# Performance work log

Measured on AMD Instinct MI355X. Metric: run time of the kernel, lower is better.

Reference implementation:

```python
import jax, jax.numpy as jnp
import numpy as np

BS = 128
HW = 128
REG = 0.1


def setup_inputs() -> dict:
    key = jax.random.key(0)
    k1, k2 = jax.random.split(key)
    x1 = jax.random.normal(k1, (BS, 1, HW, HW), dtype=jnp.float32)
    x2 = jax.random.normal(k2, (BS, 1, HW, HW), dtype=jnp.float32)
    return {"x1": x1, "x2": x2}


def _calc_psd(x):
    # x: [2*bs, H, W]
    dft = jnp.fft.fft2(x)
    avgpsd = jnp.mean((dft * jnp.conj(dft)).real, axis=0)  # [H, W]
    return jnp.mean(jnp.log(avgpsd)) - jnp.log(jnp.mean(avgpsd))


def reference(x1, x2):
    a = x1[:, 0]  # [bs, H, W] (squeeze channel)
    b = x2[:, 0]
    # pairwise Frobenius distances: Dist[i, j] = ||x1[i] - x2[j]||_F
    diff = a[:, None, :, :] - b[None, :, :, :]          # [bs, bs, H, W]
    Dist = jnp.sqrt(jnp.sum(diff * diff, axis=(-2, -1)))  # [bs, bs]
    bs = Dist.shape[0]
    # CrossEntropyLoss(Dist, arange(bs)) = mean_i(logsumexp(Dist[i]) - Dist[i, i])
    log_probs = jax.nn.log_softmax(Dist, axis=-1)
    ce = -jnp.mean(jnp.diagonal(log_probs))
    # PSD regularizer on cat(x1, x2)
    x = jnp.concatenate([a, b], axis=0)  # [2*bs, H, W]
    r = _calc_psd(x)
    return ce - REG * r
```

## Files before the change

kernel.cpp:

```cpp
#include <hip/hip_runtime.h>
#include <math.h>


#define WS_N     0
#define WS_D     256
#define WS_GP    20736
#define WS_P     4215040
#define WS_PS    6344960
#define WS_PL    6345025

#define PI_F 3.14159265358979323846f

__device__ __forceinline__ void fft128_reg(float& s0r, float& s0i,
                                           float& s1r, float& s1i,
                                           float cA, float sA,
                                           const float* wr, const float* wi,
                                           int lane) {
    float er = s0r + s1r, ei = s0i + s1i;
    float dr = s0r - s1r, di = s0i - s1i;
    float orr = dr * cA - di * sA;
    float oii = dr * sA + di * cA;
    #pragma unroll
    for (int st = 0; st < 6; ++st) {
        int m = 32 >> st;
        bool up = (lane & m) == 0;
        float tr = __shfl_xor(er, m), ti = __shfl_xor(ei, m);
        float ar = tr - er, ai = ti - ei;
        float e2r = up ? (er + tr) : (ar * wr[st] - ai * wi[st]);
        float e2i = up ? (ei + ti) : (ar * wi[st] + ai * wr[st]);
        tr = __shfl_xor(orr, m); ti = __shfl_xor(oii, m);
        float br_ = tr - orr, bi_ = ti - oii;
        float o2r = up ? (orr + tr) : (br_ * wr[st] - bi_ * wi[st]);
        float o2i = up ? (oii + ti) : (br_ * wi[st] + bi_ * wr[st]);
        er = e2r; ei = e2i; orr = o2r; oii = o2i;
    }
    s0r = er; s0i = ei; s1r = orr; s1i = oii;
}

__global__ __launch_bounds__(512) void ocl_main(const float* __restrict__ x1,
                                                const float* __restrict__ x2,
                                                float* __restrict__ ws) {
    __shared__ float4 smem4[4096];
    int t = threadIdx.x;
    int bid = blockIdx.x;

    if (bid < 256) {
        float4* As = smem4;
        float4* Bs = smem4 + 2048;
        int ks = bid, k0q = ks * 16;
        const float4* A = (const float4*)x1;
        const float4* B = (const float4*)x2;
        {
            int qi = t & 15, r0 = t >> 4;
            #pragma unroll
            for (int p = 0; p < 4; ++p) {
                int r = r0 + 32 * p;
                int sq = qi ^ ((r >> 3) & 7);
                As[r * 16 + sq] = A[(size_t)r * 4096 + k0q + qi];
                Bs[r * 16 + sq] = B[(size_t)r * 4096 + k0q + qi];
            }
        }
        __syncthreads();

        int ty = t >> 4, tx = t & 15;
        float acc[4][8];
        #pragma unroll
        for (int r = 0; r < 4; ++r)
            #pragma unroll
            for (int c = 0; c < 8; ++c) acc[r][c] = 0.0f;

        for (int qk = 0; qk < 16; ++qk) {
            float4 a4[4], b4[8];
            #pragma unroll
            for (int r = 0; r < 4; ++r) {
                int rr = ty * 4 + r;
                a4[r] = As[rr * 16 + (qk ^ ((rr >> 3) & 7))];
            }
            #pragma unroll
            for (int c = 0; c < 8; ++c) {
                int rc = tx * 8 + c;
                b4[c] = Bs[rc * 16 + (qk ^ ((rc >> 3) & 7))];
            }
            #pragma unroll
            for (int r = 0; r < 4; ++r)
                #pragma unroll
                for (int c = 0; c < 8; ++c) {
                    float4 a = a4[r], b = b4[c];
                    acc[r][c] = fmaf(a.x, b.x, fmaf(a.y, b.y,
                                fmaf(a.z, b.z, fmaf(a.w, b.w, acc[r][c]))));
                }
        }

        float4* Gp4 = (float4*)(ws + WS_GP);
        #pragma unroll
        for (int r = 0; r < 4; ++r)
            #pragma unroll
            for (int cc = 0; cc < 2; ++cc) {
                int e4 = (ty * 4 + r) * 32 + tx * 2 + cc;
                Gp4[(size_t)(e4 >> 2) * 1024 + ks * 4 + (e4 & 3)] =
                    make_float4(acc[r][cc * 4 + 0], acc[r][cc * 4 + 1],
                                acc[r][cc * 4 + 2], acc[r][cc * 4 + 3]);
            }
    } else {
        float* zre = (float*)smem4;
        float* zim = zre + 8192;
        int lane = t & 63, wave = t >> 6;
        int img = bid - 256;
        const float* src = (img < 128) ? (x1 + (size_t)img * 16384)
                                       : (x2 + (size_t)(img - 128) * 16384);

        float cA, sA, wr[6], wi[6];
        {
            float th = -PI_F * (float)lane / 64.0f;
            sA = __sinf(th); cA = __cosf(th);
            #pragma unroll
            for (int st = 0; st < 6; ++st) {
                int m = 32 >> st;
                float a = -PI_F * (float)(lane & (m - 1)) / (float)m;
                wi[st] = __sinf(a); wr[st] = __cosf(a);
            }
        }
        int rb = (int)(__brev((unsigned)lane) >> 26);

        float nrm = 0.0f;
        #pragma unroll
        for (int pi = 0; pi < 8; ++pi) {
            int p = wave * 8 + pi;
            const float* r0 = src + p * 256 + lane;
            float s0r = r0[0],   s1r = r0[64];
            float s0i = r0[128], s1i = r0[192];
            nrm += s0r * s0r + s1r * s1r + s0i * s0i + s1i * s1i;
            fft128_reg(s0r, s0i, s1r, s1i, cA, sA, wr, wi, lane);
            int f0 = (2 * rb + p) & 127;
            int f1 = (2 * rb + 1 + p) & 127;
            zre[p * 128 + f0] = s0r; zim[p * 128 + f0] = s0i;
            zre[p * 128 + f1] = s1r; zim[p * 128 + f1] = s1i;
        }
        for (int off = 32; off >= 1; off >>= 1) nrm += __shfl_xor(nrm, off);
        if (lane == 0) atomicAdd(&ws[WS_N + img], nrm);
        __syncthreads();

        int p0 = (lane >> 1), p1 = 32 + (lane >> 1);
        int par = lane & 1;
        float* P = ws + WS_P;
        for (int k = wave; k < 65; k += 8) {
            float v0r, v0i, v1r, v1i;
            if (k == 0 || k == 64) {
                int c0 = (k + p0) & 127, c1 = (k + p1) & 127;
                float Z0r = zre[p0 * 128 + c0], Z0i = zim[p0 * 128 + c0];
                float Z1r = zre[p1 * 128 + c1], Z1i = zim[p1 * 128 + c1];
                v0r = par ? Z0i : Z0r; v0i = 0.0f;
                v1r = par ? Z1i : Z1r; v1i = 0.0f;
            } else {
                int kn = 128 - k;
                int ck = (k + p0) & 127, cn = (kn + p0) & 127;
                float Zkr = zre[p0 * 128 + ck], Zki = zim[p0 * 128 + ck];
                float Znr = zre[p0 * 128 + cn], Zni = zim[p0 * 128 + cn];
                float e0r = 0.5f * (Zkr + Znr), e0i = 0.5f * (Zki - Zni);
                float q0r = 0.5f * (Zki + Zni), q0i = 0.5f * (Znr - Zkr);
                v0r = par ? q0r : e0r; v0i = par ? q0i : e0i;
                ck = (k + p1) & 127; cn = (kn + p1) & 127;
                Zkr = zre[p1 * 128 + ck]; Zki = zim[p1 * 128 + ck];
                Znr = zre[p1 * 128 + cn]; Zni = zim[p1 * 128 + cn];
                float e1r = 0.5f * (Zkr + Znr), e1i = 0.5f * (Zki - Zni);
                float q1r = 0.5f * (Zki + Zni), q1i = 0.5f * (Znr - Zkr);
                v1r = par ? q1r : e1r; v1i = par ? q1i : e1i;
            }
            fft128_reg(v0r, v0i, v1r, v1i, cA, sA, wr, wi, lane);
            int m = lane & 15, hi = lane >> 4;
            P[(size_t)(k * 8 + 0 + hi) * 4096 + img * 16 + m] = v0r * v0r + v0i * v0i;
            P[(size_t)(k * 8 + 4 + hi) * 4096 + img * 16 + m] = v1r * v1r + v1i * v1i;
        }
    }
}

__global__ __launch_bounds__(256) void ocl_finish(float* __restrict__ ws) {
    int bid = blockIdx.x, t = threadIdx.x;
    int lane = t & 63, wave = t >> 6;

    if (bid < 256) {
        int g = bid;
        const float4* Gp4 = (const float4*)(ws + WS_GP);
        int q = (lane >> 4) & 3, kg = lane & 15;
        const float4* base = Gp4 + (size_t)g * 4096 + wave * 1024 + q;
        float4 v[16];
        #pragma unroll
        for (int it = 0; it < 16; ++it) v[it] = base[(kg * 16 + it) * 4];
        float4 s = v[0];
        #pragma unroll
        for (int it = 1; it < 16; ++it) {
            s.x += v[it].x; s.y += v[it].y; s.z += v[it].z; s.w += v[it].w;
        }
        #pragma unroll
        for (int msk = 1; msk <= 8; msk <<= 1) {
            s.x += __shfl_xor(s.x, msk); s.y += __shfl_xor(s.y, msk);
            s.z += __shfl_xor(s.z, msk); s.w += __shfl_xor(s.w, msk);
        }
        if (kg == 0) {
            int i = g >> 1;
            float nai = ws[WS_N + i];
            float4 nb4 = ((const float4*)(ws + WS_N + 128))[(g & 1) * 16 + wave * 4 + q];
            float4 d;
            d.x = sqrtf(fmaxf(nai + nb4.x - 2.0f * s.x, 0.0f));
            d.y = sqrtf(fmaxf(nai + nb4.y - 2.0f * s.y, 0.0f));
            d.z = sqrtf(fmaxf(nai + nb4.z - 2.0f * s.z, 0.0f));
            d.w = sqrtf(fmaxf(nai + nb4.w - 2.0f * s.w, 0.0f));
            ((float4*)(ws + WS_D))[i * 32 + (g & 1) * 16 + wave * 4 + q] = d;
        }
    } else {
        int k = bid - 256;
        const float4* P4 = (const float4*)(ws + WS_P);
        int b16 = t >> 5, m4 = (t >> 3) & 3, hq = t & 7;
        const float4* base = P4 + (size_t)(k * 8 + b16) * 1024 + m4;
        float4 s = make_float4(0.f, 0.f, 0.f, 0.f);
        #pragma unroll
        for (int half = 0; half < 2; ++half) {
            float4 u[16];
            #pragma unroll
            for (int it = 0; it < 16; ++it)
                u[it] = base[(hq * 32 + half * 16 + it) * 4];
            #pragma unroll
            for (int it = 0; it < 16; ++it) {
                s.x += u[it].x; s.y += u[it].y; s.z += u[it].z; s.w += u[it].w;
            }
        }
        #pragma unroll
        for (int msk = 1; msk <= 4; msk <<= 1) {
            s.x += __shfl_xor(s.x, msk); s.y += __shfl_xor(s.y, msk);
            s.z += __shfl_xor(s.z, msk); s.w += __shfl_xor(s.w, msk);
        }
        float sS = 0.0f, sL = 0.0f;
        if (hq == 0) {
            float w = (k == 0 || k == 64) ? 1.0f : 2.0f;
            sS = w * (s.x + s.y + s.z + s.w);
            sL = w * (logf(s.x) + logf(s.y) + logf(s.z) + logf(s.w));
        }
        #pragma unroll
        for (int off = 32; off >= 1; off >>= 1) {
            sS += __shfl_xor(sS, off);
            sL += __shfl_xor(sL, off);
        }
        __shared__ float aS[4], aL[4];
        if (lane == 0) { aS[wave] = sS; aL[wave] = sL; }
        __syncthreads();
        if (t == 0) {
            ws[WS_PS + k] = aS[0] + aS[1] + aS[2] + aS[3];
            ws[WS_PL + k] = aL[0] + aL[1] + aL[2] + aL[3];
        }
    }
}

__global__ __launch_bounds__(256) void ocl_tail(const float* __restrict__ ws,
                                                float* __restrict__ out) {
    int t = threadIdx.x, lane = t & 63, wave = t >> 6;

    int i = t >> 1, h = t & 1;
    const float4* D4 = (const float4*)(ws + WS_D);
    float4 dv[16];
    #pragma unroll
    for (int it = 0; it < 16; ++it) dv[it] = D4[i * 32 + h * 16 + it];
    float mx = -1.0f;
    #pragma unroll
    for (int it = 0; it < 16; ++it)
        mx = fmaxf(mx, fmaxf(fmaxf(dv[it].x, dv[it].y), fmaxf(dv[it].z, dv[it].w)));
    float mo = __shfl_xor(mx, 1);
    float m2 = fmaxf(mx, mo);
    float sm = 0.0f;
    #pragma unroll
    for (int it = 0; it < 16; ++it)
        sm += __expf(dv[it].x - m2) + __expf(dv[it].y - m2) +
              __expf(dv[it].z - m2) + __expf(dv[it].w - m2);
    sm += __shfl_xor(sm, 1);
    float dii = 0.0f;
    if ((i >> 6) == h) {
        int lc = i & 63;
        float4 dq = dv[lc >> 2];
        dii = (i & 2) ? ((i & 1) ? dq.w : dq.z) : ((i & 1) ? dq.y : dq.x);
    }
    dii += __shfl_xor(dii, 1);
    float rowacc = 0.5f * (m2 + logf(sm) - dii);

    float sS = 0.0f, sL = 0.0f;
    if (t < 65) { sS = ws[WS_PS + t]; sL = ws[WS_PL + t]; }
    #pragma unroll
    for (int off = 32; off >= 1; off >>= 1) {
        sS += __shfl_xor(sS, off);
        sL += __shfl_xor(sL, off);
        rowacc += __shfl_xor(rowacc, off);
    }
    __shared__ float bS[4], bL[4], bR[4];
    if (lane == 0) { bS[wave] = sS; bL[wave] = sL; bR[wave] = rowacc; }
    __syncthreads();
    if (t == 0) {
        float S_ = bS[0] + bS[1] + bS[2] + bS[3];
        float L_ = bL[0] + bL[1] + bL[2] + bL[3];
        float R_ = bR[0] + bR[1] + bR[2] + bR[3];
        float ce = R_ / 128.0f;
        float r  = L_ / 16384.0f - logf(S_ / 16384.0f);
        out[0] = ce - 0.1f * r;
    }
}

extern "C" void kernel_launch(void* const* d_in, const int* in_sizes, int n_in,
                              void* d_out, int out_size, void* d_ws, size_t ws_size,
                              hipStream_t stream) {
    (void)in_sizes; (void)n_in; (void)out_size; (void)ws_size;
    const float* x1 = (const float*)d_in[0];
    const float* x2 = (const float*)d_in[1];
    float* ws  = (float*)d_ws;
    float* out = (float*)d_out;

    hipLaunchKernelGGL(ocl_main,   dim3(512), dim3(512), 0, stream, x1, x2, ws);
    hipLaunchKernelGGL(ocl_finish, dim3(321), dim3(256), 0, stream, ws);
    hipLaunchKernelGGL(ocl_tail,   dim3(1),   dim3(256), 0, stream, ws, out);
}
```

Baseline: 100.3 us.

## Replace norm atomics with per-wave partials and fuse partial softmax into finish

The FFT kernel now writes one squared-norm partial per wave instead of doing an atomicAdd per image, and the finish kernel sums those partials itself. The finish kernel also computes the distance tile, takes a per-block max and sum-of-exp, and records the diagonal entry. The tail kernel then only merges two partial log-sum-exp values per row. This removes the atomics, their need for a zeroed accumulator, and the tail's serial row scan over the full distance matrix. In exchange the finish blocks gain extra syncthreads and shared-memory reductions.

Result: faster. 94.28 us (-6.0%).

```diff
diff --git a/kernel.cpp b/kernel.cpp
--- a/kernel.cpp
+++ b/kernel.cpp
@@ -2,8 +2,10 @@
 #include <math.h>
 
 
-#define WS_N     0
-#define WS_D     256
+#define WS_SE    256
+#define WS_MX    512
+#define WS_DII   768
+#define WS_NP    16640
 #define WS_GP    20736
 #define WS_P     4215040
 #define WS_PS    6344960
@@ -137,7 +139,7 @@
             zre[p * 128 + f1] = s1r; zim[p * 128 + f1] = s1i;
         }
         for (int off = 32; off >= 1; off >>= 1) nrm += __shfl_xor(nrm, off);
-        if (lane == 0) atomicAdd(&ws[WS_N + img], nrm);
+        if (lane == 0) ws[WS_NP + img * 8 + wave] = nrm;
         __syncthreads();
 
         int p0 = (lane >> 1), p1 = 32 + (lane >> 1);
@@ -186,6 +188,21 @@
         float4 v[16];
         #pragma unroll
         for (int it = 0; it < 16; ++it) v[it] = base[(kg * 16 + it) * 4];
+
+        __shared__ float nbs[64];
+        __shared__ float s_na;
+        __shared__ float sm[4], sm2[4];
+        if (t < 64) {
+            const float* np = ws + WS_NP + (size_t)(128 + (g & 1) * 64 + t) * 8;
+            nbs[t] = ((np[0] + np[1]) + (np[2] + np[3])) +
+                     ((np[4] + np[5]) + (np[6] + np[7]));
+        }
+        if (t == 64) {
+            const float* np = ws + WS_NP + (size_t)(g >> 1) * 8;
+            s_na = ((np[0] + np[1]) + (np[2] + np[3])) +
+                   ((np[4] + np[5]) + (np[6] + np[7]));
+        }
+
         float4 s = v[0];
         #pragma unroll
         for (int it = 1; it < 16; ++it) {
@@ -196,16 +213,39 @@
             s.x += __shfl_xor(s.x, msk); s.y += __shfl_xor(s.y, msk);
             s.z += __shfl_xor(s.z, msk); s.w += __shfl_xor(s.w, msk);
         }
-        if (kg == 0) {
-            int i = g >> 1;
-            float nai = ws[WS_N + i];
-            float4 nb4 = ((const float4*)(ws + WS_N + 128))[(g & 1) * 16 + wave * 4 + q];
-            float4 d;
-            d.x = sqrtf(fmaxf(nai + nb4.x - 2.0f * s.x, 0.0f));
-            d.y = sqrtf(fmaxf(nai + nb4.y - 2.0f * s.y, 0.0f));
-            d.z = sqrtf(fmaxf(nai + nb4.z - 2.0f * s.z, 0.0f));
-            d.w = sqrtf(fmaxf(nai + nb4.w - 2.0f * s.w, 0.0f));
-            ((float4*)(ws + WS_D))[i * 32 + (g & 1) * 16 + wave * 4 + q] = d;
+        __syncthreads();
+
+        int cq = wave * 4 + q;
+        float nai = s_na;
+        float4 d;
+        d.x = sqrtf(fmaxf(nai + nbs[cq * 4 + 0] - 2.0f * s.x, 0.0f));
+        d.y = sqrtf(fmaxf(nai + nbs[cq * 4 + 1] - 2.0f * s.y, 0.0f));
+        d.z = sqrtf(fmaxf(nai + nbs[cq * 4 + 2] - 2.0f * s.z, 0.0f));
+        d.w = sqrtf(fmaxf(nai + nbs[cq * 4 + 3] - 2.0f * s.w, 0.0f));
+
+        int i = g >> 1;
+        int jr = i - (g & 1) * 64;
+        if (kg == 0 && jr >= 0 && jr < 64 && cq == (jr >> 2)) {
+            float dii = (jr & 2) ? ((jr & 1) ? d.w : d.z) : ((jr & 1) ? d.y : d.x);
+            ws[WS_DII + i] = dii;
+        }
+
+        float m = fmaxf(fmaxf(d.x, d.y), fmaxf(d.z, d.w));
+        m = fmaxf(m, __shfl_xor(m, 16));
+        m = fmaxf(m, __shfl_xor(m, 32));
+        if (lane == 0) sm[wave] = m;
+        __syncthreads();
+        float M = fmaxf(fmaxf(sm[0], sm[1]), fmaxf(sm[2], sm[3]));
+
+        float se = __expf(d.x - M) + __expf(d.y - M) +
+                   __expf(d.z - M) + __expf(d.w - M);
+        se += __shfl_xor(se, 16);
+        se += __shfl_xor(se, 32);
+        if (lane == 0) sm2[wave] = se;
+        __syncthreads();
+        if (t == 0) {
+            ws[WS_SE + g] = sm2[0] + sm2[1] + sm2[2] + sm2[3];
+            ws[WS_MX + g] = M;
         }
     } else {
         int k = bid - 256;
@@ -254,31 +294,16 @@
                                                 float* __restrict__ out) {
     int t = threadIdx.x, lane = t & 63, wave = t >> 6;
 
-    int i = t >> 1, h = t & 1;
-    const float4* D4 = (const float4*)(ws + WS_D);
-    float4 dv[16];
-    #pragma unroll
-    for (int it = 0; it < 16; ++it) dv[it] = D4[i * 32 + h * 16 + it];
-    float mx = -1.0f;
-    #pragma unroll
-    for (int it = 0; it < 16; ++it)
-        mx = fmaxf(mx, fmaxf(fmaxf(dv[it].x, dv[it].y), fmaxf(dv[it].z, dv[it].w)));
-    float mo = __shfl_xor(mx, 1);
-    float m2 = fmaxf(mx, mo);
-    float sm = 0.0f;
-    #pragma unroll
-    for (int it = 0; it < 16; ++it)
-        sm += __expf(dv[it].x - m2) + __expf(dv[it].y - m2) +
-              __expf(dv[it].z - m2) + __expf(dv[it].w - m2);
-    sm += __shfl_xor(sm, 1);
-    float dii = 0.0f;
-    if ((i >> 6) == h) {
-        int lc = i & 63;
-        float4 dq = dv[lc >> 2];
-        dii = (i & 2) ? ((i & 1) ? dq.w : dq.z) : ((i & 1) ? dq.y : dq.x);
-    }
-    dii += __shfl_xor(dii, 1);
-    float rowacc = 0.5f * (m2 + logf(sm) - dii);
+    float rowacc = 0.0f;
+    if (t < 128) {
+        int i = t;
+        float sea = ws[WS_SE + 2 * i],     seb = ws[WS_SE + 2 * i + 1];
+        float ma  = ws[WS_MX + 2 * i],     mb  = ws[WS_MX + 2 * i + 1];
+        float dii = ws[WS_DII + i];
+        float M = fmaxf(ma, mb);
+        float se = sea * __expf(ma - M) + seb * __expf(mb - M);
+        rowacc = M + logf(se) - dii;
+    }
 
     float sS = 0.0f, sL = 0.0f;
     if (t < 65) { sS = ws[WS_PS + t]; sL = ws[WS_PL + t]; }
```
